# Optimization experiments

Hardware: AMD Instinct MI355X
Metric: run time of the kernel (lower is better)

Reference implementation:

```python
import jax, jax.numpy as jnp
import numpy as np

N_NODES = 100000
N_EDGES = 1600000
IN_DIM, HID_DIM, OUT_DIM = 64, 128, 1


def gcn_conv(x, W, b, src, dst, n_nodes):
    """PyG-style GCNConv: h = x @ W; out = D^-1/2 (A+I) D^-1/2 h + b.
    Self-loops handled analytically (message h_i * dinv_i^2) to avoid
    concatenating them onto the edge list."""
    h = x @ W  # [N, F_out]
    ones = jnp.ones((src.shape[0],), dtype=x.dtype)
    deg = jax.ops.segment_sum(ones, dst, num_segments=n_nodes) + 1.0  # +1 self-loop
    dinv = jax.lax.rsqrt(deg)  # deg >= 1 so always finite
    norm = dinv[src] * dinv[dst]  # [E]
    msgs = h[src] * norm[:, None]  # [E, F_out] gather + scale
    agg = jax.ops.segment_sum(msgs, dst, num_segments=n_nodes)  # scatter-add
    agg = agg + h * (dinv * dinv)[:, None]  # self-loop contribution
    return agg + b


def setup_inputs() -> dict:
    key = jax.random.key(0)
    k1, k2, k3, k4 = jax.random.split(key, 4)
    x = jax.random.normal(k1, (N_NODES, IN_DIM), dtype=jnp.float32)
    edge_index = jax.random.randint(k2, (2, N_EDGES), 0, N_NODES, dtype=jnp.int64)
    # Glorot-ish init for weights
    W1 = jax.random.normal(k3, (IN_DIM, HID_DIM), dtype=jnp.float32) / np.sqrt(IN_DIM)
    b1 = jnp.zeros((HID_DIM,), dtype=jnp.float32)
    W2 = jax.random.normal(k4, (HID_DIM, OUT_DIM), dtype=jnp.float32) / np.sqrt(HID_DIM)
    b2 = jnp.zeros((OUT_DIM,), dtype=jnp.float32)
    return {"x": x, "edge_index": edge_index, "W1": W1, "b1": b1, "W2": W2, "b2": b2}


def reference(x, edge_index, W1, b1, W2, b2):
    src, dst = edge_index[0], edge_index[1]
    h = gcn_conv(x, W1, b1, src, dst, N_NODES)
    h = jax.nn.relu(h)
    # dropout(0.3) in eval mode == identity
    out = gcn_conv(h, W2, b2, src, dst, N_NODES)
    return out.reshape(-1)  # [N]
```

## Files before the change

kernel.cpp:

```cpp
#include <hip/hip_runtime.h>
#include <hip/hip_bf16.h>

#define NNODES 100000
#define NEDGES 1600000
#define IN_DIM 64
#define HID_DIM 128

#define BUKSHIFT 8
#define BUKNODES 256
#define NBUK ((NNODES + 255) >> 8)
#define BUKCAP 4608
#define CHUNK 4096
#define TILE_N 128
#define W1TS 72

#define EPACK(s, d)  ((s) | (((d) & 255) << 24))
#define ESRC(p)      ((p) & 0x00FFFFFF)
#define EDL(p)       ((int)(((unsigned)(p)) >> 24))

typedef __attribute__((ext_vector_type(8))) short short8;
typedef __attribute__((ext_vector_type(4))) float f32x4;

__device__ inline unsigned short f2bf(float f) {
    unsigned u = __float_as_uint(f);
    u += 0x7fff + ((u >> 16) & 1);
    return (unsigned short)(u >> 16);
}
__device__ inline unsigned bfpack2(float a, float b) {
    return (unsigned)f2bf(a) | ((unsigned)f2bf(b) << 16);
}
__device__ inline float bflo(unsigned u) { return __uint_as_float(u << 16); }
__device__ inline float bfhi(unsigned u) { return __uint_as_float(u & 0xffff0000u); }

__global__ __launch_bounds__(1024, 8) void k_part(const int* __restrict__ src,
                                                  const int* __restrict__ dst,
                                                  int* __restrict__ gbcur,
                                                  int* __restrict__ ebuf, int E) {
    __shared__ int stage[CHUNK];
    __shared__ unsigned short bukof[CHUNK];
    __shared__ int hist[NBUK];
    __shared__ int scanb[NBUK];
    __shared__ int basep[NBUK];
    __shared__ int sb[2][512];
    int t = threadIdx.x;
    int start = blockIdx.x * CHUNK;
    int n = E - start; if (n > CHUNK) n = CHUNK;

    if (t < NBUK) hist[t] = 0;
    __syncthreads();

    int myb[4], myr[4], mp[4];
    #pragma unroll
    for (int i = 0; i < 4; i++) {
        int c = t + i * 1024;
        if (c < n) {
            int s = src[start + c];
            int d = dst[start + c];
            int b = d >> BUKSHIFT;
            myb[i] = b;
            mp[i]  = EPACK(s, d);
            myr[i] = atomicAdd(&hist[b], 1);
        } else myb[i] = -1;
    }
    __syncthreads();

    {
        int v = (t < NBUK) ? hist[t] : 0;
        if (t < 512) sb[0][t] = v;
        __syncthreads();
        int pin = 0;
        for (int ofs = 1; ofs < 512; ofs <<= 1) {
            if (t < 512) sb[pin ^ 1][t] = (t >= ofs) ? sb[pin][t] + sb[pin][t - ofs]
                                                     : sb[pin][t];
            __syncthreads();
            pin ^= 1;
        }
        if (t < NBUK) scanb[t] = sb[pin][t] - v;
    }

    if (t < NBUK) {
        int h = hist[t];
        basep[t] = h ? (t * BUKCAP + atomicAdd(&gbcur[t], h)) : 0;
    }
    __syncthreads();

    #pragma unroll
    for (int i = 0; i < 4; i++) {
        if (myb[i] >= 0) {
            int p = scanb[myb[i]] + myr[i];
            stage[p] = mp[i];
            bukof[p] = (unsigned short)myb[i];
        }
    }
    __syncthreads();

    for (int c = t; c < n; c += 1024) {
        int b = bukof[c];
        ebuf[basep[b] + (c - scanb[b])] = stage[c];
    }
}

__global__ __launch_bounds__(1024, 8) void k_bfill(const int* __restrict__ gbcur,
                                                   const int* __restrict__ ebuf,
                                                   const float* __restrict__ x,
                                                   int* __restrict__ off,
                                                   int* __restrict__ nend,
                                                   float* __restrict__ dinv,
                                                   int* __restrict__ csr,
                                                   unsigned* __restrict__ xsb, int N) {
    __shared__ int sEdge[BUKCAP];
    __shared__ int lcnt[BUKNODES];
    __shared__ int sbuf[2][BUKNODES];
    __shared__ int cur[BUKNODES];
    __shared__ float sdinv[BUKNODES];
    int b = blockIdx.x, t = threadIdx.x;
    int nbase = b << BUKSHIFT;
    int rbase = b * BUKCAP;
    int cntb = gbcur[b];
    if (t < BUKNODES) lcnt[t] = 0;
    __syncthreads();
    for (int i = t; i < cntb; i += 1024) {
        int p = ebuf[rbase + i];
        sEdge[i] = p;
        atomicAdd(&lcnt[EDL(p)], 1);
    }
    __syncthreads();
    int v = (t < BUKNODES) ? lcnt[t] : 0;
    if (t < BUKNODES) sbuf[0][t] = v;
    __syncthreads();
    int pin = 0;
    for (int ofs = 1; ofs < BUKNODES; ofs <<= 1) {
        if (t < BUKNODES) sbuf[pin ^ 1][t] = (t >= ofs) ? sbuf[pin][t] + sbuf[pin][t - ofs]
                                                        : sbuf[pin][t];
        __syncthreads();
        pin ^= 1;
    }
    if (t < BUKNODES) {
        int o = rbase + sbuf[pin][t] - v;
        int nid = nbase + t;
        float dv = rsqrtf((float)v + 1.0f);
        sdinv[t] = dv;
        if (nid < N) {
            off[nid]  = o;
            nend[nid] = o + v;
            dinv[nid] = dv;
        }
        cur[t] = o;
    }
    __syncthreads();
    for (int i = t; i < cntb; i += 1024) {
        int p = sEdge[i];
        int pos = atomicAdd(&cur[EDL(p)], 1);
        csr[pos] = ESRC(p);
    }
    for (int i = t; i < BUKNODES * 16; i += 1024) {
        int nl = i >> 4;
        int nid = nbase + nl;
        if (nid < N) {
            float dv = sdinv[nl];
            float4 vx = ((const float4*)x)[(size_t)nid * 16 + (i & 15)];
            uint2 u;
            u.x = bfpack2(vx.x * dv, vx.y * dv);
            u.y = bfpack2(vx.z * dv, vx.w * dv);
            ((uint2*)xsb)[(size_t)nid * 16 + (i & 15)] = u;
        }
    }
}

__global__ __launch_bounds__(256) void k_gather64(const int* __restrict__ off,
                                                  const int* __restrict__ nend,
                                                  const int* __restrict__ csr,
                                                  const uint4* __restrict__ xsb,
                                                  const float* __restrict__ dinv,
                                                  uint4* __restrict__ aggb, int n_nodes) {
    int tid = blockIdx.x * 256 + threadIdx.x;
    int n = tid >> 6;
    if (n >= n_nodes) return;
    int lane = threadIdx.x & 63;
    int c = lane & 7;
    int g = lane >> 3;
    int beg = off[n], fin = nend[n];
    float dd = dinv[n];
    float f0[8] = {0, 0, 0, 0, 0, 0, 0, 0};
    float f1[8] = {0, 0, 0, 0, 0, 0, 0, 0};
    if (g == 0) {
        uint4 u = xsb[(size_t)n * 8 + c];
        f0[0] = bflo(u.x); f0[1] = bfhi(u.x); f0[2] = bflo(u.y); f0[3] = bfhi(u.y);
        f0[4] = bflo(u.z); f0[5] = bfhi(u.z); f0[6] = bflo(u.w); f0[7] = bfhi(u.w);
    }
    for (int base = beg; base < fin; base += 64) {
        int nn = fin - base; if (nn > 64) nn = 64;
        int idx = (lane < nn) ? csr[base + lane] : 0;
        int j = 0;
        for (; j + 16 <= nn; j += 16) {
            int sa = __shfl(idx, j + g);
            int sb = __shfl(idx, j + 8 + g);
            uint4 ua = xsb[(size_t)sa * 8 + c];
            uint4 ub = xsb[(size_t)sb * 8 + c];
            f0[0] += bflo(ua.x); f0[1] += bfhi(ua.x); f0[2] += bflo(ua.y); f0[3] += bfhi(ua.y);
            f0[4] += bflo(ua.z); f0[5] += bfhi(ua.z); f0[6] += bflo(ua.w); f0[7] += bfhi(ua.w);
            f1[0] += bflo(ub.x); f1[1] += bfhi(ub.x); f1[2] += bflo(ub.y); f1[3] += bfhi(ub.y);
            f1[4] += bflo(ub.z); f1[5] += bfhi(ub.z); f1[6] += bflo(ub.w); f1[7] += bfhi(ub.w);
        }
        for (; j < nn; j += 8) {
            int rem = nn - j;
            int sa = __shfl(idx, j + g);
            if (g < rem) {
                uint4 ua = xsb[(size_t)sa * 8 + c];
                f0[0] += bflo(ua.x); f0[1] += bfhi(ua.x); f0[2] += bflo(ua.y); f0[3] += bfhi(ua.y);
                f0[4] += bflo(ua.z); f0[5] += bfhi(ua.z); f0[6] += bflo(ua.w); f0[7] += bfhi(ua.w);
            }
        }
    }
    #pragma unroll
    for (int i = 0; i < 8; i++) f0[i] += f1[i];
    #pragma unroll
    for (int m = 8; m < 64; m <<= 1) {
        #pragma unroll
        for (int i = 0; i < 8; i++) f0[i] += __shfl_xor(f0[i], m);
    }
    if (g == 0) {
        uint4 r;
        r.x = bfpack2(f0[0] * dd, f0[1] * dd);
        r.y = bfpack2(f0[2] * dd, f0[3] * dd);
        r.z = bfpack2(f0[4] * dd, f0[5] * dd);
        r.w = bfpack2(f0[6] * dd, f0[7] * dd);
        aggb[(size_t)n * 8 + c] = r;
    }
}

__global__ __launch_bounds__(512) void k_mlp(const uint4* __restrict__ aggb,
                                             const float* __restrict__ W1,
                                             const float* __restrict__ b1,
                                             const float* __restrict__ W2,
                                             const float* __restrict__ dinv,
                                             float* __restrict__ zd, int n_nodes) {
    __shared__ __align__(16) unsigned short sW1t[HID_DIM * W1TS];
    __shared__ float sW2[HID_DIM];
    __shared__ float sb1[HID_DIM];
    int t = threadIdx.x;
    for (int i = t; i < IN_DIM * HID_DIM; i += 512) {
        int k = i >> 7, hid = i & 127;
        sW1t[hid * W1TS + k] = f2bf(W1[i]);
    }
    if (t < HID_DIM) { sW2[t] = W2[t]; sb1[t] = b1[t]; }
    __syncthreads();

    int node0 = blockIdx.x * TILE_N;
    int w = t >> 6;
    int lane = t & 63;
    int col = lane & 15;
    int quad = lane >> 4;

    int na = node0 + w * 16 + col;
    int nac = na < n_nodes ? na : 0;
    const short8* arow = (const short8*)(aggb + (size_t)nac * 8);
    short8 a0 = arow[quad];
    short8 a1 = arow[4 + quad];

    float zpart[4] = {0, 0, 0, 0};
    #pragma unroll
    for (int h0 = 0; h0 < 8; h0++) {
        int hid = h0 * 16 + col;
        const short8* brow = (const short8*)(sW1t + hid * W1TS);
        short8 b0 = brow[quad];
        short8 b1f = brow[4 + quad];
        f32x4 c = {0.f, 0.f, 0.f, 0.f};
        c = __builtin_amdgcn_mfma_f32_16x16x32_bf16(a0, b0, c, 0, 0, 0);
        c = __builtin_amdgcn_mfma_f32_16x16x32_bf16(a1, b1f, c, 0, 0, 0);
        float bb = sb1[hid], ww = sW2[hid];
        #pragma unroll
        for (int r = 0; r < 4; r++) {
            float v = c[r] + bb;
            zpart[r] += (v > 0.f ? v : 0.f) * ww;
        }
    }
    #pragma unroll
    for (int m = 1; m < 16; m <<= 1) {
        #pragma unroll
        for (int r = 0; r < 4; r++) zpart[r] += __shfl_xor(zpart[r], m);
    }
    if (col == 0) {
        #pragma unroll
        for (int r = 0; r < 4; r++) {
            int n = node0 + w * 16 + quad * 4 + r;
            if (n < n_nodes) zd[n] = zpart[r] * dinv[n];
        }
    }
}

__global__ __launch_bounds__(1024, 8) void k_gather1(const int* __restrict__ off,
                                                     const int* __restrict__ nend,
                                                     const int* __restrict__ csr,
                                                     const float* __restrict__ zd,
                                                     const float* __restrict__ dinv,
                                                     const float* __restrict__ b2,
                                                     float* __restrict__ out, int n_nodes) {
    int tid = blockIdx.x * 1024 + threadIdx.x;
    int n = tid >> 3;
    int l = tid & 7;
    if (n >= n_nodes) return;
    int beg = off[n], fin = nend[n];
    float a0 = 0.0f, a1 = 0.0f;
    for (int i = beg + l; i < fin; i += 16) {
        a0 += zd[csr[i]];
        int i2 = i + 8;
        if (i2 < fin) a1 += zd[csr[i2]];
    }
    float a = a0 + a1;
    a += __shfl_xor(a, 1);
    a += __shfl_xor(a, 2);
    a += __shfl_xor(a, 4);
    if (l == 0) out[n] = (a + zd[n]) * dinv[n] + b2[0];
}

extern "C" void kernel_launch(void* const* d_in, const int* in_sizes, int n_in,
                              void* d_out, int out_size, void* d_ws, size_t ws_size,
                              hipStream_t stream) {
    const float* x  = (const float*)d_in[0];
    const int*   ei = (const int*)d_in[1];
    const float* W1 = (const float*)d_in[2];
    const float* b1 = (const float*)d_in[3];
    const float* W2 = (const float*)d_in[4];
    const float* b2 = (const float*)d_in[5];
    float* out = (float*)d_out;

    const int N = NNODES;
    const int E = NEDGES;
    const int* src = ei;
    const int* dst = ei + E;

    int* gbcur = (int*)d_ws;
    int* off   = gbcur + 512;
    int* nend  = off + N;
    float* dinv = (float*)(nend + N);
    float* zd   = dinv + N;
    int* csr    = (int*)(zd + N);
    size_t o1 = ((size_t)((char*)(csr + NBUK * BUKCAP) - (char*)d_ws) + 127) & ~(size_t)127;
    unsigned* xsb = (unsigned*)((char*)d_ws + o1);
    size_t o2 = o1 + (size_t)N * 128;
    int*   ebuf = (int*)((char*)d_ws + o2);
    uint4* aggb = (uint4*)((char*)d_ws + o2);

    hipMemsetAsync(gbcur, 0, 512 * sizeof(int), stream);
    k_part<<<(E + CHUNK - 1) / CHUNK, 1024, 0, stream>>>(src, dst, gbcur, ebuf, E);
    k_bfill<<<NBUK, 1024, 0, stream>>>(gbcur, ebuf, x, off, nend, dinv, csr, xsb, N);
    k_gather64<<<(N * 64 + 255) / 256, 256, 0, stream>>>(off, nend, csr, (const uint4*)xsb,
                                                         dinv, aggb, N);
    k_mlp<<<(N + TILE_N - 1) / TILE_N, 512, 0, stream>>>(aggb, W1, b1, W2, dinv, zd, N);
    k_gather1<<<(N * 8 + 1023) / 1024, 1024, 0, stream>>>(off, nend, csr, zd, dinv, b2, out, N);
}
```

Baseline: 175.9 us.

## Fuse layer-1 neighbor gather into MLP kernel via shared-memory staging

Merges the per-node 64-wide gather-aggregate kernel and the MFMA MLP kernel into one kernel. Each wave now aggregates its 16 nodes one after another and writes the bf16 rows into a padded shared tile, which the MFMA stage then reads. This removes the round trip of the aggregated bf16 matrix through global memory and one kernel launch. In exchange, each wave handles its nodes serially, so there are fewer independent gathers in flight, and the weight-load setup is now overlapped with the gather.

```diff
diff --git a/kernel.cpp b/kernel.cpp
--- a/kernel.cpp
+++ b/kernel.cpp
@@ -13,6 +13,7 @@
 #define CHUNK 4096
 #define TILE_N 128
 #define W1TS 72
+#define SA_STRIDE 9
 
 #define EPACK(s, d)  ((s) | (((d) & 255) << 24))
 #define ESRC(p)      ((p) & 0x00FFFFFF)
@@ -167,94 +168,90 @@
     }
 }
 
-__global__ __launch_bounds__(256) void k_gather64(const int* __restrict__ off,
-                                                  const int* __restrict__ nend,
-                                                  const int* __restrict__ csr,
-                                                  const uint4* __restrict__ xsb,
-                                                  const float* __restrict__ dinv,
-                                                  uint4* __restrict__ aggb, int n_nodes) {
-    int tid = blockIdx.x * 256 + threadIdx.x;
-    int n = tid >> 6;
-    if (n >= n_nodes) return;
-    int lane = threadIdx.x & 63;
-    int c = lane & 7;
-    int g = lane >> 3;
-    int beg = off[n], fin = nend[n];
-    float dd = dinv[n];
-    float f0[8] = {0, 0, 0, 0, 0, 0, 0, 0};
-    float f1[8] = {0, 0, 0, 0, 0, 0, 0, 0};
-    if (g == 0) {
-        uint4 u = xsb[(size_t)n * 8 + c];
-        f0[0] = bflo(u.x); f0[1] = bfhi(u.x); f0[2] = bflo(u.y); f0[3] = bfhi(u.y);
-        f0[4] = bflo(u.z); f0[5] = bfhi(u.z); f0[6] = bflo(u.w); f0[7] = bfhi(u.w);
-    }
-    for (int base = beg; base < fin; base += 64) {
-        int nn = fin - base; if (nn > 64) nn = 64;
-        int idx = (lane < nn) ? csr[base + lane] : 0;
-        int j = 0;
-        for (; j + 16 <= nn; j += 16) {
-            int sa = __shfl(idx, j + g);
-            int sb = __shfl(idx, j + 8 + g);
-            uint4 ua = xsb[(size_t)sa * 8 + c];
-            uint4 ub = xsb[(size_t)sb * 8 + c];
-            f0[0] += bflo(ua.x); f0[1] += bfhi(ua.x); f0[2] += bflo(ua.y); f0[3] += bfhi(ua.y);
-            f0[4] += bflo(ua.z); f0[5] += bfhi(ua.z); f0[6] += bflo(ua.w); f0[7] += bfhi(ua.w);
-            f1[0] += bflo(ub.x); f1[1] += bfhi(ub.x); f1[2] += bflo(ub.y); f1[3] += bfhi(ub.y);
-            f1[4] += bflo(ub.z); f1[5] += bfhi(ub.z); f1[6] += bflo(ub.w); f1[7] += bfhi(ub.w);
-        }
-        for (; j < nn; j += 8) {
-            int rem = nn - j;
-            int sa = __shfl(idx, j + g);
-            if (g < rem) {
-                uint4 ua = xsb[(size_t)sa * 8 + c];
-                f0[0] += bflo(ua.x); f0[1] += bfhi(ua.x); f0[2] += bflo(ua.y); f0[3] += bfhi(ua.y);
-                f0[4] += bflo(ua.z); f0[5] += bfhi(ua.z); f0[6] += bflo(ua.w); f0[7] += bfhi(ua.w);
-            }
-        }
-    }
-    #pragma unroll
-    for (int i = 0; i < 8; i++) f0[i] += f1[i];
-    #pragma unroll
-    for (int m = 8; m < 64; m <<= 1) {
-        #pragma unroll
-        for (int i = 0; i < 8; i++) f0[i] += __shfl_xor(f0[i], m);
-    }
-    if (g == 0) {
-        uint4 r;
-        r.x = bfpack2(f0[0] * dd, f0[1] * dd);
-        r.y = bfpack2(f0[2] * dd, f0[3] * dd);
-        r.z = bfpack2(f0[4] * dd, f0[5] * dd);
-        r.w = bfpack2(f0[6] * dd, f0[7] * dd);
-        aggb[(size_t)n * 8 + c] = r;
-    }
-}
-
-__global__ __launch_bounds__(512) void k_mlp(const uint4* __restrict__ aggb,
-                                             const float* __restrict__ W1,
-                                             const float* __restrict__ b1,
-                                             const float* __restrict__ W2,
-                                             const float* __restrict__ dinv,
-                                             float* __restrict__ zd, int n_nodes) {
+__global__ __launch_bounds__(512, 4) void k_gmlp(const int* __restrict__ off,
+                                                 const int* __restrict__ nend,
+                                                 const int* __restrict__ csr,
+                                                 const uint4* __restrict__ xsb,
+                                                 const float* __restrict__ dinv,
+                                                 const float* __restrict__ W1,
+                                                 const float* __restrict__ b1,
+                                                 const float* __restrict__ W2,
+                                                 float* __restrict__ zd, int n_nodes) {
     __shared__ __align__(16) unsigned short sW1t[HID_DIM * W1TS];
     __shared__ float sW2[HID_DIM];
     __shared__ float sb1[HID_DIM];
+    __shared__ __align__(16) uint4 sA[8 * 16 * SA_STRIDE];
+
     int t = threadIdx.x;
     for (int i = t; i < IN_DIM * HID_DIM; i += 512) {
         int k = i >> 7, hid = i & 127;
         sW1t[hid * W1TS + k] = f2bf(W1[i]);
     }
     if (t < HID_DIM) { sW2[t] = W2[t]; sb1[t] = b1[t]; }
-    __syncthreads();
-
-    int node0 = blockIdx.x * TILE_N;
+
     int w = t >> 6;
     int lane = t & 63;
+    int c = lane & 7;
+    int g = lane >> 3;
+    int nbase = blockIdx.x * TILE_N + w * 16;
+
+    #pragma unroll 1
+    for (int i = 0; i < 16; i++) {
+        int n = nbase + i;
+        uint4 r = {0, 0, 0, 0};
+        if (n < n_nodes) {
+            int beg = off[n], fin = nend[n];
+            float dd = dinv[n];
+            float f0[8] = {0, 0, 0, 0, 0, 0, 0, 0};
+            float f1[8] = {0, 0, 0, 0, 0, 0, 0, 0};
+            if (g == 0) {
+                uint4 u = xsb[(size_t)n * 8 + c];
+                f0[0] = bflo(u.x); f0[1] = bfhi(u.x); f0[2] = bflo(u.y); f0[3] = bfhi(u.y);
+                f0[4] = bflo(u.z); f0[5] = bfhi(u.z); f0[6] = bflo(u.w); f0[7] = bfhi(u.w);
+            }
+            for (int base = beg; base < fin; base += 64) {
+                int nn = fin - base; if (nn > 64) nn = 64;
+                int idx = (lane < nn) ? csr[base + lane] : 0;
+                int j = 0;
+                for (; j + 16 <= nn; j += 16) {
+                    int sa = __shfl(idx, j + g);
+                    int sb = __shfl(idx, j + 8 + g);
+                    uint4 ua = xsb[(size_t)sa * 8 + c];
+                    uint4 ub = xsb[(size_t)sb * 8 + c];
+                    f0[0] += bflo(ua.x); f0[1] += bfhi(ua.x); f0[2] += bflo(ua.y); f0[3] += bfhi(ua.y);
+                    f0[4] += bflo(ua.z); f0[5] += bfhi(ua.z); f0[6] += bflo(ua.w); f0[7] += bfhi(ua.w);
+                    f1[0] += bflo(ub.x); f1[1] += bfhi(ub.x); f1[2] += bflo(ub.y); f1[3] += bfhi(ub.y);
+                    f1[4] += bflo(ub.z); f1[5] += bfhi(ub.z); f1[6] += bflo(ub.w); f1[7] += bfhi(ub.w);
+                }
+                for (; j < nn; j += 8) {
+                    int rem = nn - j;
+                    int sa = __shfl(idx, j + g);
+                    if (g < rem) {
+                        uint4 ua = xsb[(size_t)sa * 8 + c];
+                        f0[0] += bflo(ua.x); f0[1] += bfhi(ua.x); f0[2] += bflo(ua.y); f0[3] += bfhi(ua.y);
+                        f0[4] += bflo(ua.z); f0[5] += bfhi(ua.z); f0[6] += bflo(ua.w); f0[7] += bfhi(ua.w);
+                    }
+                }
+            }
+            #pragma unroll
+            for (int k = 0; k < 8; k++) f0[k] += f1[k];
+            #pragma unroll
+            for (int m = 8; m < 64; m <<= 1) {
+                #pragma unroll
+                for (int k = 0; k < 8; k++) f0[k] += __shfl_xor(f0[k], m);
+            }
+            r.x = bfpack2(f0[0] * dd, f0[1] * dd);
+            r.y = bfpack2(f0[2] * dd, f0[3] * dd);
+            r.z = bfpack2(f0[4] * dd, f0[5] * dd);
+            r.w = bfpack2(f0[6] * dd, f0[7] * dd);
+        }
+        if (g == 0) sA[w * 16 * SA_STRIDE + i * SA_STRIDE + c] = r;
+    }
+    __syncthreads();
+
     int col = lane & 15;
     int quad = lane >> 4;
-
-    int na = node0 + w * 16 + col;
-    int nac = na < n_nodes ? na : 0;
-    const short8* arow = (const short8*)(aggb + (size_t)nac * 8);
+    const short8* arow = (const short8*)&sA[w * 16 * SA_STRIDE + col * SA_STRIDE];
     short8 a0 = arow[quad];
     short8 a1 = arow[4 + quad];
 
@@ -265,13 +262,13 @@
         const short8* brow = (const short8*)(sW1t + hid * W1TS);
         short8 b0 = brow[quad];
         short8 b1f = brow[4 + quad];
-        f32x4 c = {0.f, 0.f, 0.f, 0.f};
-        c = __builtin_amdgcn_mfma_f32_16x16x32_bf16(a0, b0, c, 0, 0, 0);
-        c = __builtin_amdgcn_mfma_f32_16x16x32_bf16(a1, b1f, c, 0, 0, 0);
+        f32x4 cc = {0.f, 0.f, 0.f, 0.f};
+        cc = __builtin_amdgcn_mfma_f32_16x16x32_bf16(a0, b0, cc, 0, 0, 0);
+        cc = __builtin_amdgcn_mfma_f32_16x16x32_bf16(a1, b1f, cc, 0, 0, 0);
         float bb = sb1[hid], ww = sW2[hid];
         #pragma unroll
         for (int r = 0; r < 4; r++) {
-            float v = c[r] + bb;
+            float v = cc[r] + bb;
             zpart[r] += (v > 0.f ? v : 0.f) * ww;
         }
     }
@@ -283,7 +280,7 @@
     if (col == 0) {
         #pragma unroll
         for (int r = 0; r < 4; r++) {
-            int n = node0 + w * 16 + quad * 4 + r;
+            int n = nbase + quad * 4 + r;
             if (n < n_nodes) zd[n] = zpart[r] * dinv[n];
         }
     }
@@ -340,13 +337,11 @@
     unsigned* xsb = (unsigned*)((char*)d_ws + o1);
     size_t o2 = o1 + (size_t)N * 128;
     int*   ebuf = (int*)((char*)d_ws + o2);
-    uint4* aggb = (uint4*)((char*)d_ws + o2);
 
     hipMemsetAsync(gbcur, 0, 512 * sizeof(int), stream);
     k_part<<<(E + CHUNK - 1) / CHUNK, 1024, 0, stream>>>(src, dst, gbcur, ebuf, E);
     k_bfill<<<NBUK, 1024, 0, stream>>>(gbcur, ebuf, x, off, nend, dinv, csr, xsb, N);
-    k_gather64<<<(N * 64 + 255) / 256, 256, 0, stream>>>(off, nend, csr, (const uint4*)xsb,
-                                                         dinv, aggb, N);
-    k_mlp<<<(N + TILE_N - 1) / TILE_N, 512, 0, stream>>>(aggb, W1, b1, W2, dinv, zd, N);
+    k_gmlp<<<(N + TILE_N - 1) / TILE_N, 512, 0, stream>>>(off, nend, csr, (const uint4*)xsb,
+                                                          dinv, W1, b1, W2, zd, N);
     k_gather1<<<(N * 8 + 1023) / 1024, 1024, 0, stream>>>(off, nend, csr, zd, dinv, b2, out, N);
 }
```

Measured after the change: 185.1 us. 5.3% more time.
